# Optimization experiments

Measured on AMD Instinct MI355X. Metric: run time of the kernel, lower is better.

Reference implementation:

```python
import jax, jax.numpy as jnp
import numpy as np

B = 16          # number of point clouds in the batch
N_COARSE = 1024 # coarse points per cloud
N_FINE = 4096   # fine (skip) points per cloud
C_IN = 256
C_SKIP = 128
K = 3
EPS = 1e-16


def setup_inputs() -> dict:
    key = jax.random.key(0)
    ks = jax.random.split(key, 8)
    x = jax.random.normal(ks[0], (B * N_COARSE, C_IN), dtype=jnp.float32)
    pos = jax.random.uniform(ks[1], (B * N_COARSE, 3), dtype=jnp.float32)
    x_skip = jax.random.normal(ks[2], (B * N_FINE, C_SKIP), dtype=jnp.float32)
    pos_skip = jax.random.uniform(ks[3], (B * N_FINE, 3), dtype=jnp.float32)
    batch = jnp.repeat(jnp.arange(B, dtype=jnp.int64), N_COARSE)
    batch_skip = jnp.repeat(jnp.arange(B, dtype=jnp.int64), N_FINE)
    W1 = jax.random.normal(ks[4], (C_IN + C_SKIP, 256), dtype=jnp.float32) * (1.0 / np.sqrt(C_IN + C_SKIP))
    b1 = jnp.zeros((256,), dtype=jnp.float32)
    W2 = jax.random.normal(ks[5], (256, 256), dtype=jnp.float32) * (1.0 / np.sqrt(256))
    b2 = jnp.zeros((256,), dtype=jnp.float32)
    return {"x": x, "pos": pos, "batch": batch, "x_skip": x_skip,
            "pos_skip": pos_skip, "batch_skip": batch_skip,
            "W1": W1, "b1": b1, "W2": W2, "b2": b2}


def _knn_interpolate(x, pos, pos_skip):
    # Equal-sized clouds: reshape to [B, N, *] and do batched kNN.
    xc = x.reshape(B, N_COARSE, C_IN)
    pc = pos.reshape(B, N_COARSE, 3)
    pf = pos_skip.reshape(B, N_FINE, 3)
    # squared pairwise distances [B, M, N]
    d2 = (jnp.sum(pf * pf, -1)[:, :, None]
          + jnp.sum(pc * pc, -1)[:, None, :]
          - 2.0 * jnp.einsum('bmd,bnd->bmn', pf, pc))
    d2 = jnp.maximum(d2, 0.0)
    neg_d2k, idx = jax.lax.top_k(-d2, K)          # k smallest distances
    w = 1.0 / jnp.maximum(-neg_d2k, EPS)          # [B, M, K] inverse-sq-dist weights
    gathered = jax.vmap(lambda f, i: f[i])(xc, idx)  # [B, M, K, C]
    y = jnp.sum(w[..., None] * gathered, axis=2) / jnp.sum(w, axis=2, keepdims=True)
    return y.reshape(B * N_FINE, C_IN)


def reference(x, pos, batch, x_skip, pos_skip, batch_skip, W1, b1, W2, b2):
    x_interp = _knn_interpolate(x, pos, pos_skip)          # [B*M, C_IN]
    h = jnp.concatenate([x_interp, x_skip], axis=1)        # [B*M, C_IN + C_SKIP]
    h = jax.nn.relu(h @ W1 + b1)
    out = jax.nn.relu(h @ W2 + b2)
    return out
```

## Files before the change

### kernel.cpp

```cpp
#include <hip/hip_runtime.h>

typedef float  f32x4  __attribute__((ext_vector_type(4)));
typedef short  short8 __attribute__((ext_vector_type(8)));
typedef unsigned short ushort_t;
typedef ushort_t us4   __attribute__((ext_vector_type(4)));

#define NCOARSE 1024
#define NFINE   4096

__device__ __forceinline__ ushort_t f2bf(float f){
  union { float f; unsigned u; } a; a.f = f;
  unsigned u = a.u;
  return (ushort_t)((u + 0x7fffu + ((u >> 16) & 1u)) >> 16);
}

__device__ __forceinline__ f32x4 splat4(float v){ f32x4 t = {v, v, v, v}; return t; }

__global__ void prep_w(const float* __restrict__ W, ushort_t* __restrict__ Wp, int nelem){
  int e = blockIdx.x * 256 + threadIdx.x;
  if (e >= nelem) return;
  int j    = e & 7;
  int lane = (e >> 3) & 63;
  int g    = e >> 9;
  int nb   = g & 15;
  int kc   = g >> 4;
  int k = kc * 32 + (lane >> 4) * 8 + j;
  int n = nb * 16 + (lane & 15);
  Wp[e] = f2bf(W[k * 256 + n]);
}

__global__ __launch_bounds__(256) void knn_kernel(const float* __restrict__ pos,
                           const float* __restrict__ pos_skip,
                           int* __restrict__ knn_i, float* __restrict__ knn_w){
  __shared__ f32x4 cand[8][129];
  const int tid = threadIdx.x;
  const int b   = blockIdx.x >> 7;
  const int m   = blockIdx.x * 32 + (tid >> 3);
  const int chunk = tid & 7;

  const float* p = pos + (size_t)b * NCOARSE * 3;
  for (int c = tid; c < NCOARSE; c += 256){
    float x = p[3*c], y = p[3*c+1], z = p[3*c+2];
    float sc = __fadd_rn(__fadd_rn(__fmul_rn(x,x), __fmul_rn(y,y)), __fmul_rn(z,z));
    f32x4 v = { x, y, z, sc };
    cand[c >> 7][c & 127] = v;
  }
  __syncthreads();

  const float* q = pos_skip + (size_t)m * 3;
  float qx = q[0], qy = q[1], qz = q[2];
  float sf = __fadd_rn(__fadd_rn(__fmul_rn(qx,qx), __fmul_rn(qy,qy)), __fmul_rn(qz,qz));

  float d0 = 1e30f, d1 = 1e30f, d2 = 1e30f;
  int   i0 = 0,     i1 = 0,     i2 = 0;
  const int gbase = chunk * 128;
  #pragma unroll 4
  for (int i = 0; i < 128; ++i){
    f32x4 v = cand[chunk][i];
    float dot = __fadd_rn(__fadd_rn(__fmul_rn(qx, v.x), __fmul_rn(qy, v.y)),
                          __fmul_rn(qz, v.z));
    float d = __fsub_rn(__fadd_rn(sf, v.w), __fmul_rn(2.0f, dot));
    d = fmaxf(d, 0.0f);
    if (d < d2){
      int gi = gbase + i;
      if (d < d1){
        d2 = d1; i2 = i1;
        if (d < d0){ d1 = d0; i1 = i0; d0 = d; i0 = gi; }
        else       { d1 = d;  i1 = gi; }
      } else { d2 = d; i2 = gi; }
    }
  }

  #pragma unroll
  for (int mlev = 1; mlev <= 4; mlev <<= 1){
    float e0 = __shfl_xor(d0, mlev), e1 = __shfl_xor(d1, mlev), e2 = __shfl_xor(d2, mlev);
    int   j0 = __shfl_xor(i0, mlev), j1 = __shfl_xor(i1, mlev), j2 = __shfl_xor(i2, mlev);
    #pragma unroll
    for (int s = 0; s < 3; ++s){
      float e = (s == 0) ? e0 : (s == 1) ? e1 : e2;
      int   j = (s == 0) ? j0 : (s == 1) ? j1 : j2;
      bool l2 = (e < d2) || (e == d2 && j < i2);
      if (l2){
        bool l1 = (e < d1) || (e == d1 && j < i1);
        if (l1){
          d2 = d1; i2 = i1;
          bool l0 = (e < d0) || (e == d0 && j < i0);
          if (l0){ d1 = d0; i1 = i0; d0 = e; i0 = j; }
          else   { d1 = e;  i1 = j; }
        } else { d2 = e; i2 = j; }
      }
    }
  }

  if (chunk == 0){
    float w0 = 1.0f / fmaxf(d0, 1e-16f);
    float w1 = 1.0f / fmaxf(d1, 1e-16f);
    float w2 = 1.0f / fmaxf(d2, 1e-16f);
    float ws = __fadd_rn(__fadd_rn(w0, w1), w2);
    knn_i[3*m]   = b * NCOARSE + i0;
    knn_i[3*m+1] = b * NCOARSE + i1;
    knn_i[3*m+2] = b * NCOARSE + i2;
    knn_w[3*m]   = w0 / ws;
    knn_w[3*m+1] = w1 / ws;
    knn_w[3*m+2] = w2 / ws;
  }
}

__global__ __launch_bounds__(256, 2)
void fused_fp(const float* __restrict__ x, const float* __restrict__ x_skip,
              const int* __restrict__ knn_i, const float* __restrict__ knn_w,
              const ushort_t* __restrict__ W1p, const float* __restrict__ b1,
              const ushort_t* __restrict__ W2p, const float* __restrict__ b2,
              float* __restrict__ out){
  __shared__ ushort_t h1[64 * 384];
  __shared__ ushort_t h2[64 * 256];
  char* h1b = (char*)h1;
  char* h2b = (char*)h2;
  const int tid  = threadIdx.x;
  const int row0 = blockIdx.x * 64;

  for (int it = 0; it < 16; ++it){
    int task = it * 256 + tid;
    int r  = task >> 6;
    int c4 = task & 63;
    int m  = row0 + r;
    int i0 = knn_i[3*m], i1 = knn_i[3*m+1], i2 = knn_i[3*m+2];
    float w0 = knn_w[3*m], w1 = knn_w[3*m+1], w2 = knn_w[3*m+2];
    f32x4 v0 = ((const f32x4*)(x + (size_t)i0 * 256))[c4];
    f32x4 v1 = ((const f32x4*)(x + (size_t)i1 * 256))[c4];
    f32x4 v2 = ((const f32x4*)(x + (size_t)i2 * 256))[c4];
    f32x4 v  = v0 * w0 + v1 * w1 + v2 * w2;
    int byte = (r * 768 + c4 * 8) ^ ((r & 7) << 4);
    us4 pk = { f2bf(v.x), f2bf(v.y), f2bf(v.z), f2bf(v.w) };
    *(us4*)(h1b + byte) = pk;
  }
  for (int it = 0; it < 8; ++it){
    int task = it * 256 + tid;
    int r  = task >> 5;
    int c4 = task & 31;
    int m  = row0 + r;
    f32x4 v = ((const f32x4*)(x_skip + (size_t)m * 128))[c4];
    int byte = (r * 768 + 512 + c4 * 8) ^ ((r & 7) << 4);
    us4 pk = { f2bf(v.x), f2bf(v.y), f2bf(v.z), f2bf(v.w) };
    *(us4*)(h1b + byte) = pk;
  }
  __syncthreads();

  const int w   = tid >> 6;
  const int lane = tid & 63;
  const int lhi = lane >> 4;
  const int llo = lane & 15;

  f32x4 acc[4][4];
  #pragma unroll
  for (int nbp = 0; nbp < 4; ++nbp){
    float bb = b1[w * 64 + nbp * 16 + llo];
    #pragma unroll
    for (int mb = 0; mb < 4; ++mb) acc[mb][nbp] = splat4(bb);
  }
  #pragma unroll
  for (int kk = 0; kk < 12; ++kk){
    short8 af[4];
    #pragma unroll
    for (int mb = 0; mb < 4; ++mb){
      int r = mb * 16 + llo;
      int byte = (r * 768 + kk * 64 + lhi * 16) ^ ((r & 7) << 4);
      af[mb] = *(const short8*)(h1b + byte);
    }
    short8 bfr[4];
    #pragma unroll
    for (int nbp = 0; nbp < 4; ++nbp)
      bfr[nbp] = *(const short8*)(W1p + ((size_t)((kk * 16 + w * 4 + nbp) * 64 + lane)) * 8);
    #pragma unroll
    for (int mb = 0; mb < 4; ++mb)
      #pragma unroll
      for (int nbp = 0; nbp < 4; ++nbp)
        acc[mb][nbp] = __builtin_amdgcn_mfma_f32_16x16x32_bf16(af[mb], bfr[nbp], acc[mb][nbp], 0, 0, 0);
  }
  #pragma unroll
  for (int mb = 0; mb < 4; ++mb)
    #pragma unroll
    for (int nbp = 0; nbp < 4; ++nbp)
      #pragma unroll
      for (int rg = 0; rg < 4; ++rg){
        int r   = mb * 16 + lhi * 4 + rg;
        int col = w * 64 + nbp * 16 + llo;
        int byte = (r * 512 + col * 2) ^ ((r & 7) << 4);
        *(ushort_t*)(h2b + byte) = f2bf(fmaxf(acc[mb][nbp][rg], 0.0f));
      }
  __syncthreads();

  f32x4 acc2[4][4];
  #pragma unroll
  for (int nbp = 0; nbp < 4; ++nbp){
    float bb = b2[w * 64 + nbp * 16 + llo];
    #pragma unroll
    for (int mb = 0; mb < 4; ++mb) acc2[mb][nbp] = splat4(bb);
  }
  #pragma unroll
  for (int kk = 0; kk < 8; ++kk){
    short8 af[4];
    #pragma unroll
    for (int mb = 0; mb < 4; ++mb){
      int r = mb * 16 + llo;
      int byte = (r * 512 + kk * 64 + lhi * 16) ^ ((r & 7) << 4);
      af[mb] = *(const short8*)(h2b + byte);
    }
    short8 bfr[4];
    #pragma unroll
    for (int nbp = 0; nbp < 4; ++nbp)
      bfr[nbp] = *(const short8*)(W2p + ((size_t)((kk * 16 + w * 4 + nbp) * 64 + lane)) * 8);
    #pragma unroll
    for (int mb = 0; mb < 4; ++mb)
      #pragma unroll
      for (int nbp = 0; nbp < 4; ++nbp)
        acc2[mb][nbp] = __builtin_amdgcn_mfma_f32_16x16x32_bf16(af[mb], bfr[nbp], acc2[mb][nbp], 0, 0, 0);
  }
  #pragma unroll
  for (int mb = 0; mb < 4; ++mb)
    #pragma unroll
    for (int nbp = 0; nbp < 4; ++nbp)
      #pragma unroll
      for (int rg = 0; rg < 4; ++rg){
        int row = row0 + mb * 16 + lhi * 4 + rg;
        int col = w * 64 + nbp * 16 + llo;
        out[(size_t)row * 256 + col] = fmaxf(acc2[mb][nbp][rg], 0.0f);
      }
}

extern "C" void kernel_launch(void* const* d_in, const int* in_sizes, int n_in,
                              void* d_out, int out_size, void* d_ws, size_t ws_size,
                              hipStream_t stream){
  (void)in_sizes; (void)n_in; (void)out_size; (void)ws_size;
  const float* x        = (const float*)d_in[0];
  const float* pos      = (const float*)d_in[1];
  const float* x_skip   = (const float*)d_in[3];
  const float* pos_skip = (const float*)d_in[4];
  const float* W1 = (const float*)d_in[6];
  const float* b1 = (const float*)d_in[7];
  const float* W2 = (const float*)d_in[8];
  const float* b2 = (const float*)d_in[9];
  float* out = (float*)d_out;
  char* ws = (char*)d_ws;
  ushort_t* W1p = (ushort_t*)(ws);
  ushort_t* W2p = (ushort_t*)(ws + 196608);
  int*      ki  = (int*)(ws + 327680);
  float*    kw  = (float*)(ws + 1114112);

  hipLaunchKernelGGL(prep_w, dim3(384), dim3(256), 0, stream, W1, W1p, 98304);
  hipLaunchKernelGGL(prep_w, dim3(256), dim3(256), 0, stream, W2, W2p, 65536);
  hipLaunchKernelGGL(knn_kernel, dim3(2048), dim3(256), 0, stream, pos, pos_skip, ki, kw);
  hipLaunchKernelGGL(fused_fp, dim3(1024), dim3(256), 0, stream,
                     x, x_skip, ki, kw, W1p, b1, W2p, b2, out);
}
```

Measured before the change: 97.47 us.

## Alias LDS buffers, raise occupancy, remap blocks, restructure gather loop

The h1 and h2 shared buffers now share one allocation, with an extra barrier before h2 is written, which cuts LDS per block so three blocks can fit per CU (launch bounds raised to 3). Block indices are remapped (blockIdx & 7 << 7 | blockIdx >> 3), presumably so that blocks launched together touch different clouds and spread work across XCDs/L2. The gather is restructured so each group of 4 threads owns one row: the kNN indices and weights are loaded once per row, and the x_skip loads are issued up front into registers. The tighter register budget and the extra barrier may cost some MFMA throughput.

```diff
diff --git a/kernel.cpp b/kernel.cpp
--- a/kernel.cpp
+++ b/kernel.cpp
@@ -106,47 +106,55 @@
   }
 }
 
-__global__ __launch_bounds__(256, 2)
+__global__ __launch_bounds__(256, 3)
 void fused_fp(const float* __restrict__ x, const float* __restrict__ x_skip,
               const int* __restrict__ knn_i, const float* __restrict__ knn_w,
               const ushort_t* __restrict__ W1p, const float* __restrict__ b1,
               const ushort_t* __restrict__ W2p, const float* __restrict__ b2,
               float* __restrict__ out){
-  __shared__ ushort_t h1[64 * 384];
-  __shared__ ushort_t h2[64 * 256];
-  char* h1b = (char*)h1;
-  char* h2b = (char*)h2;
+  __shared__ ushort_t hbuf[64 * 384];
+  char* h1b = (char*)hbuf;
+  char* h2b = (char*)hbuf;
   const int tid  = threadIdx.x;
-  const int row0 = blockIdx.x * 64;
-
-  for (int it = 0; it < 16; ++it){
-    int task = it * 256 + tid;
-    int r  = task >> 6;
-    int c4 = task & 63;
-    int m  = row0 + r;
+  const int lb   = ((blockIdx.x & 7) << 7) + (blockIdx.x >> 3);
+  const int row0 = lb * 64;
+
+  {
+    const int r   = tid >> 2;
+    const int sub = tid & 3;
+    const int m   = row0 + r;
+
+    const f32x4* xsr = (const f32x4*)(x_skip + (size_t)m * 128);
+    f32x4 xs[8];
+    #pragma unroll
+    for (int it = 0; it < 8; ++it) xs[it] = xsr[it * 4 + sub];
+
     int i0 = knn_i[3*m], i1 = knn_i[3*m+1], i2 = knn_i[3*m+2];
     float w0 = knn_w[3*m], w1 = knn_w[3*m+1], w2 = knn_w[3*m+2];
-    f32x4 v0 = ((const f32x4*)(x + (size_t)i0 * 256))[c4];
-    f32x4 v1 = ((const f32x4*)(x + (size_t)i1 * 256))[c4];
-    f32x4 v2 = ((const f32x4*)(x + (size_t)i2 * 256))[c4];
-    f32x4 v  = v0 * w0 + v1 * w1 + v2 * w2;
-    int byte = (r * 768 + c4 * 8) ^ ((r & 7) << 4);
-    us4 pk = { f2bf(v.x), f2bf(v.y), f2bf(v.z), f2bf(v.w) };
-    *(us4*)(h1b + byte) = pk;
-  }
-  for (int it = 0; it < 8; ++it){
-    int task = it * 256 + tid;
-    int r  = task >> 5;
-    int c4 = task & 31;
-    int m  = row0 + r;
-    f32x4 v = ((const f32x4*)(x_skip + (size_t)m * 128))[c4];
-    int byte = (r * 768 + 512 + c4 * 8) ^ ((r & 7) << 4);
-    us4 pk = { f2bf(v.x), f2bf(v.y), f2bf(v.z), f2bf(v.w) };
-    *(us4*)(h1b + byte) = pk;
-  }
-  __syncthreads();
-
-  const int w   = tid >> 6;
+    const f32x4* x0 = (const f32x4*)(x + (size_t)i0 * 256);
+    const f32x4* x1 = (const f32x4*)(x + (size_t)i1 * 256);
+    const f32x4* x2 = (const f32x4*)(x + (size_t)i2 * 256);
+
+    #pragma unroll
+    for (int it = 0; it < 16; ++it){
+      int c4 = it * 4 + sub;
+      f32x4 v = x0[c4] * w0 + x1[c4] * w1 + x2[c4] * w2;
+      int byte = (r * 768 + c4 * 8) ^ ((r & 7) << 4);
+      us4 pk = { f2bf(v.x), f2bf(v.y), f2bf(v.z), f2bf(v.w) };
+      *(us4*)(h1b + byte) = pk;
+    }
+    #pragma unroll
+    for (int it = 0; it < 8; ++it){
+      int c4 = it * 4 + sub;
+      f32x4 v = xs[it];
+      int byte = (r * 768 + 512 + c4 * 8) ^ ((r & 7) << 4);
+      us4 pk = { f2bf(v.x), f2bf(v.y), f2bf(v.z), f2bf(v.w) };
+      *(us4*)(h1b + byte) = pk;
+    }
+  }
+  __syncthreads();
+
+  const int wp  = tid >> 6;
   const int lane = tid & 63;
   const int lhi = lane >> 4;
   const int llo = lane & 15;
@@ -154,7 +162,7 @@
   f32x4 acc[4][4];
   #pragma unroll
   for (int nbp = 0; nbp < 4; ++nbp){
-    float bb = b1[w * 64 + nbp * 16 + llo];
+    float bb = b1[wp * 64 + nbp * 16 + llo];
     #pragma unroll
     for (int mb = 0; mb < 4; ++mb) acc[mb][nbp] = splat4(bb);
   }
@@ -170,13 +178,15 @@
     short8 bfr[4];
     #pragma unroll
     for (int nbp = 0; nbp < 4; ++nbp)
-      bfr[nbp] = *(const short8*)(W1p + ((size_t)((kk * 16 + w * 4 + nbp) * 64 + lane)) * 8);
+      bfr[nbp] = *(const short8*)(W1p + ((size_t)((kk * 16 + wp * 4 + nbp) * 64 + lane)) * 8);
     #pragma unroll
     for (int mb = 0; mb < 4; ++mb)
       #pragma unroll
       for (int nbp = 0; nbp < 4; ++nbp)
         acc[mb][nbp] = __builtin_amdgcn_mfma_f32_16x16x32_bf16(af[mb], bfr[nbp], acc[mb][nbp], 0, 0, 0);
   }
+  __syncthreads();
+
   #pragma unroll
   for (int mb = 0; mb < 4; ++mb)
     #pragma unroll
@@ -184,7 +194,7 @@
       #pragma unroll
       for (int rg = 0; rg < 4; ++rg){
         int r   = mb * 16 + lhi * 4 + rg;
-        int col = w * 64 + nbp * 16 + llo;
+        int col = wp * 64 + nbp * 16 + llo;
         int byte = (r * 512 + col * 2) ^ ((r & 7) << 4);
         *(ushort_t*)(h2b + byte) = f2bf(fmaxf(acc[mb][nbp][rg], 0.0f));
       }
@@ -193,7 +203,7 @@
   f32x4 acc2[4][4];
   #pragma unroll
   for (int nbp = 0; nbp < 4; ++nbp){
-    float bb = b2[w * 64 + nbp * 16 + llo];
+    float bb = b2[wp * 64 + nbp * 16 + llo];
     #pragma unroll
     for (int mb = 0; mb < 4; ++mb) acc2[mb][nbp] = splat4(bb);
   }
@@ -209,7 +219,7 @@
     short8 bfr[4];
     #pragma unroll
     for (int nbp = 0; nbp < 4; ++nbp)
-      bfr[nbp] = *(const short8*)(W2p + ((size_t)((kk * 16 + w * 4 + nbp) * 64 + lane)) * 8);
+      bfr[nbp] = *(const short8*)(W2p + ((size_t)((kk * 16 + wp * 4 + nbp) * 64 + lane)) * 8);
     #pragma unroll
     for (int mb = 0; mb < 4; ++mb)
       #pragma unroll
@@ -223,7 +233,7 @@
       #pragma unroll
       for (int rg = 0; rg < 4; ++rg){
         int row = row0 + mb * 16 + lhi * 4 + rg;
-        int col = w * 64 + nbp * 16 + llo;
+        int col = wp * 64 + nbp * 16 + llo;
         out[(size_t)row * 256 + col] = fmaxf(acc2[mb][nbp][rg], 0.0f);
       }
 }
```

Result: faster. 88.03 us (-9.7%).
